# Kernel tuning notes

Hardware: AMD Instinct MI355X
Metric: run time of the kernel (lower is better)

The kernel has to match this reference:

```python
import jax, jax.numpy as jnp
import numpy as np

# Complete binary tree: B trees, L leaves each, processed level-synchronously.
B, L, IN_DIM, MEM = 64, 1024, 300, 256


def setup_inputs() -> dict:
    key = jax.random.key(0)
    ks = jax.random.split(key, 6)
    s = 0.05
    embs = jax.random.normal(ks[0], (B, L, IN_DIM), dtype=jnp.float32)
    # Leaf module: c = cx(x); h = sigmoid(ox(x)) * tanh(c)
    Wcx = jax.random.normal(ks[1], (MEM, IN_DIM), dtype=jnp.float32) * s
    bcx = jnp.zeros((MEM,), jnp.float32)
    Wox = jax.random.normal(ks[2], (MEM, IN_DIM), dtype=jnp.float32) * s
    box = jnp.zeros((MEM,), jnp.float32)
    # Composer: 4 gates (i, lf, rf, u), each gate = Linear(lh) + Linear(rh).
    # Stacked: Wl/Wr have shape [4, MEM, MEM]; biases [4, MEM].
    Wl = jax.random.normal(ks[3], (4, MEM, MEM), dtype=jnp.float32) * s
    bl = jnp.zeros((4, MEM), jnp.float32)
    Wr = jax.random.normal(ks[4], (4, MEM, MEM), dtype=jnp.float32) * s
    br = jnp.zeros((4, MEM), jnp.float32)
    return dict(embs=embs, Wcx=Wcx, bcx=bcx, Wox=Wox, box=box,
                Wl=Wl, bl=bl, Wr=Wr, br=br)


def reference(embs, Wcx, bcx, Wox, box, Wl, bl, Wr, br):
    # Leaf module (BinaryTreeLeafModule.forward), vectorized over all leaves.
    c = jnp.einsum('blx,mx->blm', embs, Wcx) + bcx          # [B, L, MEM]
    o = jax.nn.sigmoid(jnp.einsum('blx,mx->blm', embs, Wox) + box)
    h = o * jnp.tanh(c)

    bias = bl + br                                          # [4, MEM]
    n = c.shape[1]
    while n > 1:  # log2(L) levels, static unrolled loop
        lc, rc = c[:, 0::2], c[:, 1::2]                     # [B, n/2, MEM]
        lh, rh = h[:, 0::2], h[:, 1::2]
        # All 4 gate pre-activations fused: [B, n/2, 4, MEM]
        g = (jnp.einsum('bnm,gom->bngo', lh, Wl)
             + jnp.einsum('bnm,gom->bngo', rh, Wr) + bias)
        i = jax.nn.sigmoid(g[..., 0, :])
        lf = jax.nn.sigmoid(g[..., 1, :])
        rf = jax.nn.sigmoid(g[..., 2, :])
        u = jnp.tanh(g[..., 3, :])
        c = i * u + lf * lc + rf * rc                       # composer cell
        h = jnp.tanh(c)                                     # gate_output=False path
        n //= 2

    # Root state (tree.state = (c, h)); stacked as [2, B, MEM]
    return jnp.stack([c[:, 0], h[:, 0]])
```

## Files before the change

### kernel.cpp

```cpp
#include <hip/hip_runtime.h>
#include <hip/hip_bf16.h>
#include <hip/hip_fp16.h>


typedef __attribute__((ext_vector_type(8))) short bf16x8;
typedef __attribute__((ext_vector_type(4))) float f32x4;

__device__ __forceinline__ float fsig(float x)  { return 1.f / (1.f + __expf(-x)); }
__device__ __forceinline__ float ftanh(float x) { return 1.f - 2.f / (__expf(2.f * x) + 1.f); }
__device__ __forceinline__ ushort f2bf(float x) {
    __hip_bfloat16 b = __float2bfloat16(x);
    return *reinterpret_cast<ushort*>(&b);
}

__device__ __forceinline__ void gld_lds16(const void* g, void* l) {
    __builtin_amdgcn_global_load_lds((const __attribute__((address_space(1))) void*)g,
                                     (__attribute__((address_space(3))) void*)l, 16, 0, 0);
}

__global__ void prep(const float* __restrict__ Wl,  const float* __restrict__ Wr,
                     const float* __restrict__ bl,  const float* __restrict__ br,
                     const float* __restrict__ Wcx, const float* __restrict__ Wox,
                     const float* __restrict__ bcx, const float* __restrict__ box,
                     const float* __restrict__ embs,
                     ushort* __restrict__ Wb2, ushort* __restrict__ WbL,
                     float* __restrict__ bp2, float* __restrict__ bpL,
                     ushort* __restrict__ embsB)
{
    const int gid = blockIdx.x * 256 + threadIdx.x;
    for (int i = gid; i < 524288; i += 262144) {
        int e = i & 7, slot = (i >> 3) & 3, o = (i >> 5) & 255;
        int g = (i >> 13) & 3, t = i >> 15;
        int q = slot ^ ((o >> 1) & 3);
        int k = t * 32 + q * 8 + e;
        float v = (k < 256) ? Wl[(g * 256 + o) * 256 + k]
                            : Wr[(g * 256 + o) * 256 + (k - 256)];
        Wb2[i] = f2bf(v);
    }
    if (gid < 163840) {
        int e = gid & 7, slot = (gid >> 3) & 3, o = (gid >> 5) & 255;
        int g = (gid >> 13) & 1, t = gid >> 14;
        int q = slot ^ ((o >> 1) & 3);
        int k = t * 32 + q * 8 + e;
        float v = 0.f;
        if (k < 300) v = g ? Wox[o * 300 + k] : Wcx[o * 300 + k];
        WbL[gid] = f2bf(v);
    }
    if (gid < 1024) bp2[gid] = bl[gid] + br[gid];
    if (gid < 512) {
        int g = gid >> 8, o = gid & 255;
        bpL[gid] = g ? box[o] : bcx[o];
    }
    for (int i = gid; i < 65536 * 80; i += 262144) {
        int row = i / 80;
        int k = (i - row * 80) * 4;
        float4 v = make_float4(0.f, 0.f, 0.f, 0.f);
        if (k < 300) v = *(const float4*)(embs + (size_t)row * 300 + k);
        ushort4 o4;
        o4.x = f2bf(v.x); o4.y = f2bf(v.y); o4.z = f2bf(v.z); o4.w = f2bf(v.w);
        *(ushort4*)(embsB + (size_t)row * 320 + k) = o4;
    }
}


template<int NG, int HALVES, int MODE>
__global__ __launch_bounds__(256, 4)
void mfma_gemm(const ushort* __restrict__ A,
               const ushort* __restrict__ Wb,
               const float* __restrict__ bp,
               const __half* __restrict__ Cprev,
               __half* __restrict__ c_out,
               ushort* __restrict__ h_out,
               float* __restrict__ fout,
               int M)
{
    constexpr int K = HALVES * 32;
    constexpr int OW = 128 / NG;
    __shared__ __align__(16) ushort As[2][512 * 8];
    __shared__ __align__(16) ushort Bs[2][512 * 8];

    const int tid = threadIdx.x;
    const int wid = tid >> 6, ln = tid & 63;
    const int lq = ln >> 4, lr = ln & 15;
    const int wm = wid >> 1, wn = wid & 1;
    const int rowBlk = blockIdx.x * 128;
    const int o0 = blockIdx.y * OW;

    f32x4 acc[4][4];
#pragma unroll
    for (int m = 0; m < 4; ++m)
#pragma unroll
        for (int f = 0; f < 4; ++f) acc[m][f] = f32x4{0.f, 0.f, 0.f, 0.f};

    const int ar0 = tid >> 2,  as0 = tid & 3;
    const int ar1 = ar0 + 64;
    const int aq0 = (as0 - ((ar0 >> 1) & 3)) & 3;
    const int aq1 = (as0 - ((ar1 >> 1) & 3)) & 3;
    const ushort* aP0 = A + (size_t)min(rowBlk + ar0, M - 1) * K + aq0 * 8;
    const ushort* aP1 = A + (size_t)min(rowBlk + ar1, M - 1) * K + aq1 * 8;
    const int bj0 = tid >> 2,        bs0 = tid & 3;
    const int bj1 = (tid + 256) >> 2;
    const int bg0 = bj0 / OW, bo0 = o0 + (bj0 & (OW - 1));
    const int bg1 = bj1 / OW, bo1 = o0 + (bj1 & (OW - 1));
    const ushort* bP0 = Wb + ((size_t)bg0 * 1024 + bo0 * 4 + bs0) * 8;
    const ushort* bP1 = Wb + ((size_t)bg1 * 1024 + bo1 * 4 + bs0) * 8;
    constexpr size_t BSTR = (size_t)NG * 1024 * 8;

    const int aSw = (lq + ((lr >> 1) & 3)) & 3;
    const int bSw = lq ^ ((lr >> 1) & 3);
    int aOff[4];
#pragma unroll
    for (int m = 0; m < 4; ++m)
        aOff[m] = ((wm * 64 + m * 16 + lr) * 4 + aSw) * 8;
    int bOff[4];
#pragma unroll
    for (int f = 0; f < 4; ++f)
        bOff[f] = ((f * 32 + wn * 16 + lr) * 4 + bSw) * 8;

    gld_lds16(aP0, &As[0][tid * 8]);
    gld_lds16(aP1, &As[0][(tid + 256) * 8]);
    gld_lds16(bP0, &Bs[0][tid * 8]);
    gld_lds16(bP1, &Bs[0][(tid + 256) * 8]);

#pragma unroll
    for (int h = 0; h < HALVES; ++h) {
        __syncthreads();
        const int cur = h & 1;
        if (h + 1 < HALVES) {
            gld_lds16(aP0 + (size_t)(h + 1) * 32, &As[cur ^ 1][tid * 8]);
            gld_lds16(aP1 + (size_t)(h + 1) * 32, &As[cur ^ 1][(tid + 256) * 8]);
            gld_lds16(bP0 + (size_t)(h + 1) * BSTR, &Bs[cur ^ 1][tid * 8]);
            gld_lds16(bP1 + (size_t)(h + 1) * BSTR, &Bs[cur ^ 1][(tid + 256) * 8]);
        }
        bf16x8 a[4];
#pragma unroll
        for (int m = 0; m < 4; ++m)
            a[m] = *(const bf16x8*)&As[cur][aOff[m]];
#pragma unroll
        for (int f = 0; f < 4; ++f) {
            bf16x8 b = *(const bf16x8*)&Bs[cur][bOff[f]];
#pragma unroll
            for (int m = 0; m < 4; ++m)
                acc[m][f] = __builtin_amdgcn_mfma_f32_16x16x32_bf16(a[m], b, acc[m][f], 0, 0, 0);
        }
    }

#pragma unroll
    for (int m = 0; m < 4; ++m) {
        const int row0 = rowBlk + wm * 64 + m * 16 + lq * 4;
        if constexpr (MODE == 0) {
#pragma unroll
            for (int ob = 0; ob < 2; ++ob) {
                const int col = o0 + ob * 32 + wn * 16 + lr;
                const float bc = bp[col], bo = bp[256 + col];
#pragma unroll
                for (int j = 0; j < 4; ++j) {
                    int row = row0 + j;
                    if (row < M) {
                        float cv = acc[m][ob][j] + bc;
                        float ov = acc[m][2 + ob][j] + bo;
                        c_out[(size_t)row * 256 + col] = __float2half(cv);
                        h_out[(size_t)row * 256 + col] = f2bf(fsig(ov) * ftanh(cv));
                    }
                }
            }
        } else {
            const int col = o0 + wn * 16 + lr;
            const float bi  = bp[col],       blf = bp[256 + col];
            const float brf = bp[512 + col], bu  = bp[768 + col];
#pragma unroll
            for (int j = 0; j < 4; ++j) {
                int row = row0 + j;
                if (row < M) {
                    float gi = fsig(acc[m][0][j] + bi);
                    float lf = fsig(acc[m][1][j] + blf);
                    float rf = fsig(acc[m][2][j] + brf);
                    float gu = ftanh(acc[m][3][j] + bu);
                    float lc = __half2float(Cprev[(size_t)row * 512 + col]);
                    float rc = __half2float(Cprev[(size_t)row * 512 + 256 + col]);
                    float cv = gi * gu + lf * lc + rf * rc;
                    float hv = ftanh(cv);
                    if constexpr (MODE == 2) {
                        fout[(size_t)row * 256 + col] = cv;
                        fout[16384 + (size_t)row * 256 + col] = hv;
                    } else {
                        c_out[(size_t)row * 256 + col] = __float2half(cv);
                        h_out[(size_t)row * 256 + col] = f2bf(hv);
                    }
                }
            }
        }
    }
}


extern "C" void kernel_launch(void* const* d_in, const int* in_sizes, int n_in,
                              void* d_out, int out_size, void* d_ws, size_t ws_size,
                              hipStream_t stream)
{
    const float* embs = (const float*)d_in[0];
    const float* Wcx  = (const float*)d_in[1];
    const float* bcx  = (const float*)d_in[2];
    const float* Wox  = (const float*)d_in[3];
    const float* box  = (const float*)d_in[4];
    const float* Wl   = (const float*)d_in[5];
    const float* bl   = (const float*)d_in[6];
    const float* Wr   = (const float*)d_in[7];
    const float* br   = (const float*)d_in[8];

    char* p = (char*)d_ws;
    ushort* Wb2 = (ushort*)p;  p += (size_t)524288 * 2;
    ushort* WbL = (ushort*)p;  p += (size_t)163840 * 2;
    float*  bp2 = (float*)p;   p += 1024 * 4;
    float*  bpL = (float*)p;   p += 512 * 4;
    __half* c0  = (__half*)p;  p += (size_t)65536 * 256 * 2;
    ushort* h0  = (ushort*)p;  p += (size_t)65536 * 256 * 2;
    char* X = p;
    ushort* embsB = (ushort*)X;
    __half* cA = (__half*)X;
    ushort* hA = (ushort*)(X + (size_t)16 * 1024 * 1024);
    __half* cB = (__half*)(X + (size_t)32 * 1024 * 1024);
    ushort* hB = (ushort*)(X + (size_t)40 * 1024 * 1024);

    prep<<<1024, 256, 0, stream>>>(Wl, Wr, bl, br, Wcx, Wox, bcx, box, embs,
                                   Wb2, WbL, bp2, bpL, embsB);

    mfma_gemm<2, 10, 0><<<dim3(512, 4), 256, 0, stream>>>(
        embsB, WbL, bpL, nullptr, c0, h0, nullptr, 65536);

    const ushort* hin = h0;
    const __half* cin = c0;
    __half* cping[2] = {cA, cB};
    ushort* hping[2] = {hA, hB};
    int flip = 0;
    for (int np = 512; np >= 1; np >>= 1) {
        int M = 64 * np;
        int gx = (M + 127) / 128;
        if (np == 1) {
            mfma_gemm<4, 16, 2><<<dim3(gx, 8), 256, 0, stream>>>(
                hin, Wb2, bp2, cin, nullptr, nullptr, (float*)d_out, M);
        } else {
            __half* co = cping[flip]; ushort* ho = hping[flip];
            mfma_gemm<4, 16, 1><<<dim3(gx, 8), 256, 0, stream>>>(
                hin, Wb2, bp2, cin, co, ho, nullptr, M);
            cin = co; hin = ho; flip ^= 1;
        }
    }
}
```

Before: 287.1 us.

## Fuse last six tree levels into one persistent kernel with grid barriers

```diff
diff --git a/kernel.cpp b/kernel.cpp
--- a/kernel.cpp
+++ b/kernel.cpp
@@ -2,6 +2,8 @@
 #include <hip/hip_bf16.h>
 #include <hip/hip_fp16.h>
 
+
+#define TB 128
 
 typedef __attribute__((ext_vector_type(8))) short bf16x8;
 typedef __attribute__((ext_vector_type(4))) float f32x4;
@@ -16,6 +18,19 @@
 __device__ __forceinline__ void gld_lds16(const void* g, void* l) {
     __builtin_amdgcn_global_load_lds((const __attribute__((address_space(1))) void*)g,
                                      (__attribute__((address_space(3))) void*)l, 16, 0, 0);
+}
+
+__device__ __forceinline__ void grid_barrier(unsigned* ctr, int b) {
+    __syncthreads();
+    if (threadIdx.x == 0) {
+        __threadfence();
+        __hip_atomic_fetch_add(ctr + b, 1u, __ATOMIC_ACQ_REL, __HIP_MEMORY_SCOPE_AGENT);
+        while (__hip_atomic_load(ctr + b, __ATOMIC_ACQUIRE, __HIP_MEMORY_SCOPE_AGENT)
+               < (unsigned)TB)
+            __builtin_amdgcn_s_sleep(8);
+        __threadfence();
+    }
+    __syncthreads();
 }
 
 __global__ void prep(const float* __restrict__ Wl,  const float* __restrict__ Wr,
@@ -62,7 +77,6 @@
     }
 }
 
-
 template<int NG, int HALVES, int MODE>
 __global__ __launch_bounds__(256, 4)
 void mfma_gemm(const ushort* __restrict__ A,
@@ -71,7 +85,6 @@
                const __half* __restrict__ Cprev,
                __half* __restrict__ c_out,
                ushort* __restrict__ h_out,
-               float* __restrict__ fout,
                int M)
 {
     constexpr int K = HALVES * 32;
@@ -179,16 +192,111 @@
                     float lc = __half2float(Cprev[(size_t)row * 512 + col]);
                     float rc = __half2float(Cprev[(size_t)row * 512 + 256 + col]);
                     float cv = gi * gu + lf * lc + rf * rc;
+                    c_out[(size_t)row * 256 + col] = __float2half(cv);
+                    h_out[(size_t)row * 256 + col] = f2bf(ftanh(cv));
+                }
+            }
+        }
+    }
+}
+
+
+__global__ __launch_bounds__(512, 1)
+void coop_tail(const ushort* __restrict__ hIn,
+               const __half* __restrict__ cIn,
+               const ushort* __restrict__ Wb,
+               const float* __restrict__ bp,
+               ushort* __restrict__ hT0, __half* __restrict__ cT0,
+               ushort* __restrict__ hT1, __half* __restrict__ cT1,
+               float* __restrict__ dout, unsigned* __restrict__ ctr)
+{
+    __shared__ __align__(16) ushort W[65536];
+
+    const int tid = threadIdx.x;
+    const int wid = tid >> 6, ln = tid & 63;
+    const int lq = ln >> 4, lr = ln & 15;
+    const int og = blockIdx.x & 7, rg = blockIdx.x >> 3;
+    const int o0 = og * 32;
+
+#pragma unroll
+    for (int s = 0; s < 16; ++s) {
+        int c = tid + 512 * s;
+        int ksg = c >> 7, rem = c & 127, i = rem >> 2, sl = rem & 3;
+        gld_lds16(Wb + ((size_t)ksg * 1024 + (o0 + i) * 4 + sl) * 8, &W[c * 8]);
+    }
+    asm volatile("s_waitcnt vmcnt(0)" ::: "memory");
+    __syncthreads();
+
+    float bias[2][4];
+#pragma unroll
+    for (int nf = 0; nf < 2; ++nf)
+#pragma unroll
+        for (int g = 0; g < 4; ++g)
+            bias[nf][g] = bp[g * 256 + o0 + nf * 16 + lr];
+    const int swz = lq ^ ((lr >> 1) & 3);
+
+    const ushort* hi = hIn;  const __half* ci = cIn;
+    ushort* hoA = hT0; __half* coA = cT0;
+    ushort* hoB = hT1; __half* coB = cT1;
+
+#pragma unroll 1
+    for (int lvl = 0; lvl < 6; ++lvl) {
+        const int npo = 32 >> lvl;
+        const int F = npo * 4;
+        const int f = rg + 16 * wid;
+        if (f < F) {
+            f32x4 acc[2][4];
+#pragma unroll
+            for (int nf = 0; nf < 2; ++nf)
+#pragma unroll
+                for (int g = 0; g < 4; ++g) acc[nf][g] = f32x4{0.f, 0.f, 0.f, 0.f};
+
+            const ushort* arow = hi + (size_t)(f * 16 + lr) * 512 + lq * 8;
+            bf16x8 a0 = *(const bf16x8*)arow;
+#pragma unroll
+            for (int ks = 0; ks < 16; ++ks) {
+                bf16x8 an;
+                if (ks + 1 < 16) an = *(const bf16x8*)(arow + (ks + 1) * 32);
+#pragma unroll
+                for (int nf = 0; nf < 2; ++nf)
+#pragma unroll
+                    for (int g = 0; g < 4; ++g) {
+                        bf16x8 b = *(const bf16x8*)
+                            &W[(((ks * 4 + g) * 128) + (nf * 16 + lr) * 4 + swz) * 8];
+                        acc[nf][g] = __builtin_amdgcn_mfma_f32_16x16x32_bf16(a0, b, acc[nf][g], 0, 0, 0);
+                    }
+                a0 = an;
+            }
+
+#pragma unroll
+            for (int nf = 0; nf < 2; ++nf) {
+                const int o = o0 + nf * 16 + lr;
+#pragma unroll
+                for (int j = 0; j < 4; ++j) {
+                    int row = f * 16 + lq * 4 + j;
+                    float gi = fsig(acc[nf][0][j] + bias[nf][0]);
+                    float lf = fsig(acc[nf][1][j] + bias[nf][1]);
+                    float rf = fsig(acc[nf][2][j] + bias[nf][2]);
+                    float gu = ftanh(acc[nf][3][j] + bias[nf][3]);
+                    float lc = __half2float(ci[(size_t)(2 * row) * 256 + o]);
+                    float rc = __half2float(ci[(size_t)(2 * row + 1) * 256 + o]);
+                    float cv = gi * gu + lf * lc + rf * rc;
                     float hv = ftanh(cv);
-                    if constexpr (MODE == 2) {
-                        fout[(size_t)row * 256 + col] = cv;
-                        fout[16384 + (size_t)row * 256 + col] = hv;
+                    if (lvl == 5) {
+                        dout[row * 256 + o] = cv;
+                        dout[16384 + row * 256 + o] = hv;
                     } else {
-                        c_out[(size_t)row * 256 + col] = __float2half(cv);
-                        h_out[(size_t)row * 256 + col] = f2bf(hv);
+                        coA[(size_t)row * 256 + o] = __float2half(cv);
+                        hoA[(size_t)row * 256 + o] = f2bf(hv);
                     }
                 }
             }
+        }
+        if (lvl < 5) {
+            grid_barrier(ctr, lvl);
+            hi = hoA; ci = coA;
+            ushort* th = hoA; hoA = hoB; hoB = th;
+            __half* tc = coA; coA = coB; coB = tc;
         }
     }
 }
@@ -209,6 +317,7 @@
     const float* br   = (const float*)d_in[8];
 
     char* p = (char*)d_ws;
+    unsigned* ctr = (unsigned*)p;  p += 256;
     ushort* Wb2 = (ushort*)p;  p += (size_t)524288 * 2;
     ushort* WbL = (ushort*)p;  p += (size_t)163840 * 2;
     float*  bp2 = (float*)p;   p += 1024 * 4;
@@ -221,29 +330,29 @@
     ushort* hA = (ushort*)(X + (size_t)16 * 1024 * 1024);
     __half* cB = (__half*)(X + (size_t)32 * 1024 * 1024);
     ushort* hB = (ushort*)(X + (size_t)40 * 1024 * 1024);
+    char* T = X + (size_t)48 * 1024 * 1024;
+    ushort* hT0 = (ushort*)T;
+    __half* cT0 = (__half*)(T + (size_t)1 * 1024 * 1024);
+    ushort* hT1 = (ushort*)(T + (size_t)2 * 1024 * 1024);
+    __half* cT1 = (__half*)(T + (size_t)2560 * 1024);
+
+    hipMemsetAsync(ctr, 0, 256, stream);
 
     prep<<<1024, 256, 0, stream>>>(Wl, Wr, bl, br, Wcx, Wox, bcx, box, embs,
                                    Wb2, WbL, bp2, bpL, embsB);
 
     mfma_gemm<2, 10, 0><<<dim3(512, 4), 256, 0, stream>>>(
-        embsB, WbL, bpL, nullptr, c0, h0, nullptr, 65536);
-
-    const ushort* hin = h0;
-    const __half* cin = c0;
-    __half* cping[2] = {cA, cB};
-    ushort* hping[2] = {hA, hB};
-    int flip = 0;
-    for (int np = 512; np >= 1; np >>= 1) {
-        int M = 64 * np;
-        int gx = (M + 127) / 128;
-        if (np == 1) {
-            mfma_gemm<4, 16, 2><<<dim3(gx, 8), 256, 0, stream>>>(
-                hin, Wb2, bp2, cin, nullptr, nullptr, (float*)d_out, M);
-        } else {
-            __half* co = cping[flip]; ushort* ho = hping[flip];
-            mfma_gemm<4, 16, 1><<<dim3(gx, 8), 256, 0, stream>>>(
-                hin, Wb2, bp2, cin, co, ho, nullptr, M);
-            cin = co; hin = ho; flip ^= 1;
-        }
-    }
-}
+        embsB, WbL, bpL, nullptr, c0, h0, 65536);
+
+    mfma_gemm<4, 16, 1><<<dim3(256, 8), 256, 0, stream>>>(
+        h0, Wb2, bp2, c0, cA, hA, 32768);
+    mfma_gemm<4, 16, 1><<<dim3(128, 8), 256, 0, stream>>>(
+        hA, Wb2, bp2, cA, cB, hB, 16384);
+    mfma_gemm<4, 16, 1><<<dim3(64, 8), 256, 0, stream>>>(
+        hB, Wb2, bp2, cB, cA, hA, 8192);
+    mfma_gemm<4, 16, 1><<<dim3(32, 8), 256, 0, stream>>>(
+        hA, Wb2, bp2, cA, cB, hB, 4096);
+
+    coop_tail<<<TB, 512, 0, stream>>>(
+        hB, cB, Wb2, bp2, hT0, cT0, hT1, cT1, (float*)d_out, ctr);
+}
```

New measurement: 297.5 us. 3.6% more time.
